# Kernel optimization log

Measured on AMD Instinct MI355X. Metric: run time of the kernel, lower is better.

Reference implementation:

```python
import jax, jax.numpy as jnp
import numpy as np

B, D, H = 524288, 256, 4
DH = D // H
LN_EPS = 1e-5


def setup_inputs() -> dict:
    key = jax.random.key(0)
    ks = jax.random.split(key, 3)
    s = 0.02  # typical init scale
    return {
        "x": jax.random.normal(ks[0], (B, 2, D), dtype=jnp.float32),
        "in_proj_w": jax.random.normal(ks[1], (3 * D, D), dtype=jnp.float32) * s,
        "in_proj_b": jnp.zeros((3 * D,), dtype=jnp.float32),
        "out_proj_w": jax.random.normal(ks[2], (D, D), dtype=jnp.float32) * s,
        "out_proj_b": jnp.zeros((D,), dtype=jnp.float32),
        "ln_gamma": jnp.ones((D,), dtype=jnp.float32),
        "ln_beta": jnp.zeros((D,), dtype=jnp.float32),
    }


def _mha_1to1(q, k, v, Wq, bq, Wk, bk, Wv, bv, Wo, bo):
    # q, k, v: [B, D]  (seq_len == 1 collapsed). Faithful MHA math.
    Q = (q @ Wq.T + bq).reshape(-1, H, DH)  # [B,H,DH]
    K = (k @ Wk.T + bk).reshape(-1, H, DH)
    V = (v @ Wv.T + bv).reshape(-1, H, DH)
    scores = jnp.sum(Q * K, axis=-1, keepdims=True) / np.sqrt(DH)  # [B,H,1]
    w = jax.nn.softmax(scores, axis=-1)  # softmax over a single key -> 1
    out = (w * V).reshape(-1, D)  # [B,D]
    return out @ Wo.T + bo


def reference(x, in_proj_w, in_proj_b, out_proj_w, out_proj_b, ln_gamma, ln_beta):
    Wq, Wk, Wv = jnp.split(in_proj_w, 3, axis=0)
    bq, bk, bv = jnp.split(in_proj_b, 3, axis=0)
    x0, x1 = x[:, 0, :], x[:, 1, :]
    out12 = _mha_1to1(x0, x1, x1, Wq, bq, Wk, bk, Wv, bv, out_proj_w, out_proj_b)
    out21 = _mha_1to1(x1, x0, x0, Wq, bq, Wk, bk, Wv, bv, out_proj_w, out_proj_b)
    fused = jnp.stack([out12, out21], axis=1)  # [B,2,D]
    y = x + fused  # dropout = identity in eval
    mu = jnp.mean(y, axis=-1, keepdims=True)
    var = jnp.var(y, axis=-1, keepdims=True)
    return (y - mu) * jax.lax.rsqrt(var + LN_EPS) * ln_gamma + ln_beta
```

## Files before the change

### kernel.cpp

```cpp
#include <hip/hip_runtime.h>

#define DD 256
#define TOTROWS (524288 * 2)
#define NBLOCKS 256
#define RPI 64
#define ITERS (TOTROWS / (NBLOCKS * RPI))
#define XROW 528
#define YROW 1040
#define XB0 0
#define XB1 (RPI * XROW)
#define YB (2 * RPI * XROW)
#define SUMS (YB + RPI * YROW)
#define MURS (SUMS + RPI * 8 * 8)
#define LDS_TOTAL (MURS + RPI * 8)

typedef __attribute__((ext_vector_type(8))) short short8;
typedef __attribute__((ext_vector_type(4))) float f32x4;
typedef __attribute__((ext_vector_type(2))) float f32x2;
typedef __attribute__((ext_vector_type(4))) unsigned short u16x4;

__device__ inline unsigned short f2bf(float x) {
    unsigned u = __builtin_bit_cast(unsigned, x);
    u += 0x7fffu + ((u >> 16) & 1u);
    return (unsigned short)(u >> 16);
}
__device__ inline float bf2f(unsigned short h) {
    unsigned u = ((unsigned)h) << 16;
    return __builtin_bit_cast(float, u);
}

__global__ void wprep_kernel(const float* __restrict__ in_w,
                             const float* __restrict__ in_b,
                             const float* __restrict__ out_w,
                             const float* __restrict__ out_b,
                             unsigned short* __restrict__ Wbf,
                             float* __restrict__ cvec) {
    __shared__ float worow[DD];
    __shared__ float part[DD];
    const int i = blockIdx.x;
    const int j = threadIdx.x;
    worow[j] = out_w[i * DD + j];
    __syncthreads();
    const float* wv = in_w + 512 * DD;
    float s = 0.f;
    for (int k = 0; k < DD; ++k) s = fmaf(worow[k], wv[k * DD + j], s);
    Wbf[i * DD + j] = f2bf(s);
    part[j] = worow[j] * in_b[512 + j];
    __syncthreads();
    if (j == 0) {
        float c = out_b[i];
        for (int k = 0; k < DD; ++k) c += part[k];
        cvec[i] = c;
    }
}

__global__ __launch_bounds__(512, 2) void fused_kernel(
    const float* __restrict__ x, const unsigned short* __restrict__ Wbf,
    const float* __restrict__ cvec, const float* __restrict__ gamma,
    const float* __restrict__ beta, float* __restrict__ out) {
    extern __shared__ __align__(16) char lds[];
    const int tid = threadIdx.x;
    const int w = tid >> 6, lane = tid & 63;
    const int m = lane & 15, g = lane >> 4;

    short8 af[2][8];
#pragma unroll
    for (int n2 = 0; n2 < 2; ++n2)
#pragma unroll
        for (int s = 0; s < 8; ++s)
            af[n2][s] = *(const short8*)(Wbf + (w * 32 + n2 * 16 + m) * 256 + s * 32 + g * 8);

    f32x4 creg[2], greg[2], breg[2];
#pragma unroll
    for (int n2 = 0; n2 < 2; ++n2) {
        const int c0 = w * 32 + n2 * 16 + g * 4;
        creg[n2] = *(const f32x4*)(cvec + c0);
        greg[n2] = *(const f32x4*)(gamma + c0);
        breg[n2] = *(const f32x4*)(beta + c0);
    }

    const size_t rowbase = (size_t)blockIdx.x * (ITERS * RPI);

    f32x4 sv[8];
#pragma unroll
    for (int j = 0; j < 8; ++j)
        sv[j] = *(const f32x4*)(x + rowbase * DD + j * 2048 + tid * 4);
#pragma unroll
    for (int j = 0; j < 8; ++j) {
        const int row = j * 8 + w;
        u16x4 h = {f2bf(sv[j][0]), f2bf(sv[j][1]), f2bf(sv[j][2]), f2bf(sv[j][3])};
        *(u16x4*)(lds + XB0 + row * XROW + lane * 8) = h;
    }
    __syncthreads();

    for (int it = 0; it < ITERS; ++it) {
        const int xb = (it & 1) ? XB1 : XB0;
        const int xn = (it & 1) ? XB0 : XB1;
        const size_t r0 = rowbase + (size_t)it * RPI;

        if (it + 1 < ITERS) {
#pragma unroll
            for (int j = 0; j < 8; ++j)
                sv[j] = *(const f32x4*)(x + (r0 + RPI) * DD + j * 2048 + tid * 4);
        }

        f32x4 acc[4][2];
#pragma unroll
        for (int t = 0; t < 4; ++t) {
            acc[t][0] = f32x4{0.f, 0.f, 0.f, 0.f};
            acc[t][1] = f32x4{0.f, 0.f, 0.f, 0.f};
        }
#pragma unroll
        for (int t = 0; t < 4; ++t) {
            const int rowp = t * 16 + (m ^ 1);
            const char* bbase = lds + xb + rowp * XROW + g * 16;
            short8 bf_[8];
#pragma unroll
            for (int s = 0; s < 8; ++s) bf_[s] = *(const short8*)(bbase + s * 64);
#pragma unroll
            for (int s = 0; s < 8; ++s) {
                acc[t][0] = __builtin_amdgcn_mfma_f32_16x16x32_bf16(af[0][s], bf_[s], acc[t][0], 0, 0, 0);
                acc[t][1] = __builtin_amdgcn_mfma_f32_16x16x32_bf16(af[1][s], bf_[s], acc[t][1], 0, 0, 0);
            }
        }

#pragma unroll
        for (int t = 0; t < 4; ++t) {
            const int rowm = t * 16 + m;
            float s1 = 0.f, s2 = 0.f;
#pragma unroll
            for (int n2 = 0; n2 < 2; ++n2) {
                u16x4 rh = *(const u16x4*)(lds + xb + rowm * XROW + w * 64 + n2 * 32 + g * 8);
                f32x4 y = acc[t][n2];
#pragma unroll
                for (int i = 0; i < 4; ++i) y[i] += bf2f(rh[i]) + creg[n2][i];
                acc[t][n2] = y;
#pragma unroll
                for (int i = 0; i < 4; ++i) {
                    s1 += y[i];
                    s2 = fmaf(y[i], y[i], s2);
                }
            }
            s1 += __shfl_xor(s1, 16); s2 += __shfl_xor(s2, 16);
            s1 += __shfl_xor(s1, 32); s2 += __shfl_xor(s2, 32);
            if (g == 0) *(f32x2*)(lds + SUMS + (rowm * 8 + w) * 8) = f32x2{s1, s2};
        }
        __syncthreads();

        {
            const int r = tid >> 3, w2 = tid & 7;
            f32x2 p = *(const f32x2*)(lds + SUMS + (r * 8 + w2) * 8);
            float a = p[0], b = p[1];
            a += __shfl_xor(a, 1); b += __shfl_xor(b, 1);
            a += __shfl_xor(a, 2); b += __shfl_xor(b, 2);
            a += __shfl_xor(a, 4); b += __shfl_xor(b, 4);
            if (w2 == 0) {
                const float mu = a * (1.f / 256.f);
                const float var = b * (1.f / 256.f) - mu * mu;
                *(f32x2*)(lds + MURS + r * 8) = f32x2{mu, rsqrtf(var + 1e-5f)};
            }
        }
        __syncthreads();

#pragma unroll
        for (int t = 0; t < 4; ++t) {
            const int rowm = t * 16 + m;
            f32x2 mr = *(const f32x2*)(lds + MURS + rowm * 8);
#pragma unroll
            for (int n2 = 0; n2 < 2; ++n2) {
                f32x4 y = acc[t][n2], o;
#pragma unroll
                for (int i = 0; i < 4; ++i)
                    o[i] = fmaf((y[i] - mr[0]) * mr[1], greg[n2][i], breg[n2][i]);
                *(f32x4*)(lds + YB + rowm * YROW + w * 128 + n2 * 64 + g * 16) = o;
            }
        }

        if (it + 1 < ITERS) {
#pragma unroll
            for (int j = 0; j < 8; ++j) {
                const int row = j * 8 + w;
                u16x4 h = {f2bf(sv[j][0]), f2bf(sv[j][1]), f2bf(sv[j][2]), f2bf(sv[j][3])};
                *(u16x4*)(lds + xn + row * XROW + lane * 8) = h;
            }
        }
        __syncthreads();

#pragma unroll
        for (int j = 0; j < 8; ++j) {
            const int row = j * 8 + w;
            f32x4 v = *(const f32x4*)(lds + YB + row * YROW + lane * 16);
            *(f32x4*)(out + (r0 + row) * DD + lane * 4) = v;
        }
    }
}

extern "C" void kernel_launch(void* const* d_in, const int* in_sizes, int n_in,
                              void* d_out, int out_size, void* d_ws, size_t ws_size,
                              hipStream_t stream) {
    const float* x     = (const float*)d_in[0];
    const float* in_w  = (const float*)d_in[1];
    const float* in_b  = (const float*)d_in[2];
    const float* out_w = (const float*)d_in[3];
    const float* out_b = (const float*)d_in[4];
    const float* gamma = (const float*)d_in[5];
    const float* beta  = (const float*)d_in[6];
    float* out = (float*)d_out;

    unsigned short* Wbf = (unsigned short*)d_ws;
    float* cvec = (float*)((char*)d_ws + 131072);

    hipLaunchKernelGGL(wprep_kernel, dim3(256), dim3(256), 0, stream,
                       in_w, in_b, out_w, out_b, Wbf, cvec);

    hipFuncSetAttribute(reinterpret_cast<const void*>(fused_kernel),
                        hipFuncAttributeMaxDynamicSharedMemorySize, LDS_TOTAL);
    hipLaunchKernelGGL(fused_kernel, dim3(NBLOCKS), dim3(512), LDS_TOTAL, stream,
                       x, Wbf, cvec, gamma, beta, out);
}
```

Baseline: 442.9 us.

## Defer LayerNorm to next iteration with per-row stats from bf16 LDS buffer

The pre-norm residual sum is now stored as bf16 in a double-buffered LDS region. LayerNorm for tile i runs at the start of iteration i+1, with each row handled by 8 lanes that reduce by shuffle and write straight to global. This removes the cross-wave partial-sum exchange and two of the three block barriers per iteration, and lets the output stores overlap the next tile's MFMA work. The cost is rounding y to bf16 before normalization, which lowers accuracy, plus an epilogue for the last tile and more registers for gamma and beta.

```diff
diff --git a/kernel.cpp b/kernel.cpp
--- a/kernel.cpp
+++ b/kernel.cpp
@@ -6,17 +6,12 @@
 #define RPI 64
 #define ITERS (TOTROWS / (NBLOCKS * RPI))
 #define XROW 528
-#define YROW 1040
-#define XB0 0
-#define XB1 (RPI * XROW)
-#define YB (2 * RPI * XROW)
-#define SUMS (YB + RPI * YROW)
-#define MURS (SUMS + RPI * 8 * 8)
-#define LDS_TOTAL (MURS + RPI * 8)
+#define XBUF(i) ((i) * (RPI * XROW))
+#define YBUF(i) (2 * RPI * XROW + (i) * (RPI * XROW))
+#define LDS_TOTAL (4 * RPI * XROW)
 
 typedef __attribute__((ext_vector_type(8))) short short8;
 typedef __attribute__((ext_vector_type(4))) float f32x4;
-typedef __attribute__((ext_vector_type(2))) float f32x2;
 typedef __attribute__((ext_vector_type(4))) unsigned short u16x4;
 
 __device__ inline unsigned short f2bf(float x) {
@@ -62,6 +57,7 @@
     const int tid = threadIdx.x;
     const int w = tid >> 6, lane = tid & 63;
     const int m = lane & 15, g = lane >> 4;
+    const int lc = lane & 7, lr = lane >> 3;
 
     short8 af[2][8];
 #pragma unroll
@@ -70,13 +66,15 @@
         for (int s = 0; s < 8; ++s)
             af[n2][s] = *(const short8*)(Wbf + (w * 32 + n2 * 16 + m) * 256 + s * 32 + g * 8);
 
-    f32x4 creg[2], greg[2], breg[2];
-#pragma unroll
-    for (int n2 = 0; n2 < 2; ++n2) {
-        const int c0 = w * 32 + n2 * 16 + g * 4;
-        creg[n2] = *(const f32x4*)(cvec + c0);
-        greg[n2] = *(const f32x4*)(gamma + c0);
-        breg[n2] = *(const f32x4*)(beta + c0);
+    f32x4 creg[2];
+#pragma unroll
+    for (int n2 = 0; n2 < 2; ++n2)
+        creg[n2] = *(const f32x4*)(cvec + w * 32 + n2 * 16 + g * 4);
+    f32x4 gg[8], bb[8];
+#pragma unroll
+    for (int k = 0; k < 8; ++k) {
+        gg[k] = *(const f32x4*)(gamma + lc * 4 + k * 32);
+        bb[k] = *(const f32x4*)(beta + lc * 4 + k * 32);
     }
 
     const size_t rowbase = (size_t)blockIdx.x * (ITERS * RPI);
@@ -89,19 +87,54 @@
     for (int j = 0; j < 8; ++j) {
         const int row = j * 8 + w;
         u16x4 h = {f2bf(sv[j][0]), f2bf(sv[j][1]), f2bf(sv[j][2]), f2bf(sv[j][3])};
-        *(u16x4*)(lds + XB0 + row * XROW + lane * 8) = h;
+        *(u16x4*)(lds + XBUF(0) + row * XROW + lane * 8) = h;
     }
     __syncthreads();
 
     for (int it = 0; it < ITERS; ++it) {
-        const int xb = (it & 1) ? XB1 : XB0;
-        const int xn = (it & 1) ? XB0 : XB1;
+        const int xbc = XBUF(it & 1);
+        const int xbn = XBUF((it + 1) & 1);
+        const int ybA = YBUF(it & 1);
+        const int ybB = YBUF((it + 1) & 1);
         const size_t r0 = rowbase + (size_t)it * RPI;
 
         if (it + 1 < ITERS) {
 #pragma unroll
             for (int j = 0; j < 8; ++j)
                 sv[j] = *(const f32x4*)(x + (r0 + RPI) * DD + j * 2048 + tid * 4);
+        }
+
+        if (it > 0) {
+            const size_t rp = r0 - RPI + w * 8 + lr;
+            u16x4 yh[8];
+#pragma unroll
+            for (int k = 0; k < 8; ++k)
+                yh[k] = *(const u16x4*)(lds + ybB + (w * 8 + lr) * XROW + lc * 8 + k * 64);
+            float s1 = 0.f, s2 = 0.f;
+            float f[8][4];
+#pragma unroll
+            for (int k = 0; k < 8; ++k)
+#pragma unroll
+                for (int e = 0; e < 4; ++e) {
+                    float v = bf2f(yh[k][e]);
+                    f[k][e] = v;
+                    s1 += v;
+                    s2 = fmaf(v, v, s2);
+                }
+            s1 += __shfl_xor(s1, 1); s2 += __shfl_xor(s2, 1);
+            s1 += __shfl_xor(s1, 2); s2 += __shfl_xor(s2, 2);
+            s1 += __shfl_xor(s1, 4); s2 += __shfl_xor(s2, 4);
+            const float mu = s1 * (1.f / 256.f);
+            const float var = s2 * (1.f / 256.f) - mu * mu;
+            const float rs = rsqrtf(var + 1e-5f);
+#pragma unroll
+            for (int k = 0; k < 8; ++k) {
+                f32x4 o;
+#pragma unroll
+                for (int e = 0; e < 4; ++e)
+                    o[e] = fmaf((f[k][e] - mu) * rs, gg[k][e], bb[k][e]);
+                *(f32x4*)(out + rp * DD + lc * 4 + k * 32) = o;
+            }
         }
 
         f32x4 acc[4][2];
@@ -113,66 +146,25 @@
 #pragma unroll
         for (int t = 0; t < 4; ++t) {
             const int rowp = t * 16 + (m ^ 1);
-            const char* bbase = lds + xb + rowp * XROW + g * 16;
-            short8 bf_[8];
-#pragma unroll
-            for (int s = 0; s < 8; ++s) bf_[s] = *(const short8*)(bbase + s * 64);
+            const char* bbase = lds + xbc + rowp * XROW + g * 16;
 #pragma unroll
             for (int s = 0; s < 8; ++s) {
-                acc[t][0] = __builtin_amdgcn_mfma_f32_16x16x32_bf16(af[0][s], bf_[s], acc[t][0], 0, 0, 0);
-                acc[t][1] = __builtin_amdgcn_mfma_f32_16x16x32_bf16(af[1][s], bf_[s], acc[t][1], 0, 0, 0);
-            }
-        }
-
+                short8 bf_ = *(const short8*)(bbase + s * 64);
+                acc[t][0] = __builtin_amdgcn_mfma_f32_16x16x32_bf16(af[0][s], bf_, acc[t][0], 0, 0, 0);
+                acc[t][1] = __builtin_amdgcn_mfma_f32_16x16x32_bf16(af[1][s], bf_, acc[t][1], 0, 0, 0);
+            }
+        }
 #pragma unroll
         for (int t = 0; t < 4; ++t) {
             const int rowm = t * 16 + m;
-            float s1 = 0.f, s2 = 0.f;
 #pragma unroll
             for (int n2 = 0; n2 < 2; ++n2) {
-                u16x4 rh = *(const u16x4*)(lds + xb + rowm * XROW + w * 64 + n2 * 32 + g * 8);
+                u16x4 rh = *(const u16x4*)(lds + xbc + rowm * XROW + w * 64 + n2 * 32 + g * 8);
                 f32x4 y = acc[t][n2];
 #pragma unroll
                 for (int i = 0; i < 4; ++i) y[i] += bf2f(rh[i]) + creg[n2][i];
-                acc[t][n2] = y;
-#pragma unroll
-                for (int i = 0; i < 4; ++i) {
-                    s1 += y[i];
-                    s2 = fmaf(y[i], y[i], s2);
-                }
-            }
-            s1 += __shfl_xor(s1, 16); s2 += __shfl_xor(s2, 16);
-            s1 += __shfl_xor(s1, 32); s2 += __shfl_xor(s2, 32);
-            if (g == 0) *(f32x2*)(lds + SUMS + (rowm * 8 + w) * 8) = f32x2{s1, s2};
-        }
-        __syncthreads();
-
-        {
-            const int r = tid >> 3, w2 = tid & 7;
-            f32x2 p = *(const f32x2*)(lds + SUMS + (r * 8 + w2) * 8);
-            float a = p[0], b = p[1];
-            a += __shfl_xor(a, 1); b += __shfl_xor(b, 1);
-            a += __shfl_xor(a, 2); b += __shfl_xor(b, 2);
-            a += __shfl_xor(a, 4); b += __shfl_xor(b, 4);
-            if (w2 == 0) {
-                const float mu = a * (1.f / 256.f);
-                const float var = b * (1.f / 256.f) - mu * mu;
-                *(f32x2*)(lds + MURS + r * 8) = f32x2{mu, rsqrtf(var + 1e-5f)};
-            }
-        }
-        __syncthreads();
-
-#pragma unroll
-        for (int t = 0; t < 4; ++t) {
-            const int rowm = t * 16 + m;
-            f32x2 mr = *(const f32x2*)(lds + MURS + rowm * 8);
-#pragma unroll
-            for (int n2 = 0; n2 < 2; ++n2) {
-                f32x4 y = acc[t][n2], o;
-#pragma unroll
-                for (int i = 0; i < 4; ++i)
-                    o[i] = fmaf((y[i] - mr[0]) * mr[1], greg[n2][i], breg[n2][i]);
-                *(f32x4*)(lds + YB + rowm * YROW + w * 128 + n2 * 64 + g * 16) = o;
+                u16x4 hy = {f2bf(y[0]), f2bf(y[1]), f2bf(y[2]), f2bf(y[3])};
+                *(u16x4*)(lds + ybA + rowm * XROW + w * 64 + n2 * 32 + g * 8) = hy;
             }
         }
 
@@ -181,16 +173,43 @@
             for (int j = 0; j < 8; ++j) {
                 const int row = j * 8 + w;
                 u16x4 h = {f2bf(sv[j][0]), f2bf(sv[j][1]), f2bf(sv[j][2]), f2bf(sv[j][3])};
-                *(u16x4*)(lds + xn + row * XROW + lane * 8) = h;
+                *(u16x4*)(lds + xbn + row * XROW + lane * 8) = h;
             }
         }
         __syncthreads();
-
-#pragma unroll
-        for (int j = 0; j < 8; ++j) {
-            const int row = j * 8 + w;
-            f32x4 v = *(const f32x4*)(lds + YB + row * YROW + lane * 16);
-            *(f32x4*)(out + (r0 + row) * DD + lane * 4) = v;
+    }
+
+    {
+        const int ybB = YBUF((ITERS - 1) & 1);
+        const size_t rp = rowbase + (size_t)(ITERS - 1) * RPI + w * 8 + lr;
+        u16x4 yh[8];
+#pragma unroll
+        for (int k = 0; k < 8; ++k)
+            yh[k] = *(const u16x4*)(lds + ybB + (w * 8 + lr) * XROW + lc * 8 + k * 64);
+        float s1 = 0.f, s2 = 0.f;
+        float f[8][4];
+#pragma unroll
+        for (int k = 0; k < 8; ++k)
+#pragma unroll
+            for (int e = 0; e < 4; ++e) {
+                float v = bf2f(yh[k][e]);
+                f[k][e] = v;
+                s1 += v;
+                s2 = fmaf(v, v, s2);
+            }
+        s1 += __shfl_xor(s1, 1); s2 += __shfl_xor(s2, 1);
+        s1 += __shfl_xor(s1, 2); s2 += __shfl_xor(s2, 2);
+        s1 += __shfl_xor(s1, 4); s2 += __shfl_xor(s2, 4);
+        const float mu = s1 * (1.f / 256.f);
+        const float var = s2 * (1.f / 256.f) - mu * mu;
+        const float rs = rsqrtf(var + 1e-5f);
+#pragma unroll
+        for (int k = 0; k < 8; ++k) {
+            f32x4 o;
+#pragma unroll
+            for (int e = 0; e < 4; ++e)
+                o[e] = fmaf((f[k][e] - mu) * rs, gg[k][e], bb[k][e]);
+            *(f32x4*)(out + rp * DD + lc * 4 + k * 32) = o;
         }
     }
 }
```

Result: no change. 439.2 us (-0.8%).
